# Kernel optimization log

Hardware: AMD Instinct MI355X
Metric: run time of the kernel (lower is better)

Reference implementation:

```python
import jax, jax.numpy as jnp
import numpy as np

NUM_MIXTURES = 10
DIM_INPUT = 512
DIM_FEATURES = 512
SEQ_LEN = 512
BATCH = 16
NUM_CHAR = 1024
DIM_CONTEXT = 256


def setup_inputs() -> dict:
    key = jax.random.key(0)
    ks = jax.random.split(key, 6)
    inputs = jax.random.normal(ks[0], (SEQ_LEN, BATCH, DIM_INPUT), dtype=jnp.float32)
    context_vectors = jax.random.normal(ks[1], (NUM_CHAR, BATCH, DIM_CONTEXT), dtype=jnp.float32)
    init_means = jnp.zeros((BATCH, NUM_MIXTURES), dtype=jnp.float32)
    # StackedLinearLayers params: 2 layers, leaky_relu between, out dim = 3*K
    s1 = 1.0 / np.sqrt(DIM_INPUT)
    s2 = 1.0 / np.sqrt(DIM_FEATURES)
    W1 = jax.random.uniform(ks[2], (DIM_INPUT, DIM_FEATURES), jnp.float32, -s1, s1)
    b1 = jax.random.uniform(ks[3], (DIM_FEATURES,), jnp.float32, -s1, s1)
    W2 = jax.random.uniform(ks[4], (DIM_FEATURES, 3 * NUM_MIXTURES), jnp.float32, -s2, s2)
    b2 = jax.random.uniform(ks[5], (3 * NUM_MIXTURES,), jnp.float32, -s2, s2)
    return dict(inputs=inputs, context_vectors=context_vectors, init_means=init_means,
                W1=W1, b1=b1, W2=W2, b2=b2, extra_chars=0)


def reference(inputs, context_vectors, init_means, W1, b1, W2, b2, extra_chars):
    K = NUM_MIXTURES
    seq_len, batch, _ = inputs.shape
    num_char = context_vectors.shape[0]
    total_char = num_char + extra_chars

    # StackedLinearLayers: leaky_relu MLP, last layer linear -> (S, B, 3K)
    h = jax.nn.leaky_relu(inputs @ W1 + b1, negative_slope=0.01)
    outs = h @ W2 + b2
    outs = jax.nn.softplus(outs)  # pos_fun = softplus

    delta_means, vars_, weights = jnp.split(outs, 3, axis=2)  # each (S, B, K)
    delta_means = delta_means / 25.0
    vars_ = jnp.clip(vars_, 0.01, 100.0)
    means = jnp.cumsum(delta_means, axis=0) + init_means[None, :, :]  # (S, B, K)

    cidxs = jnp.arange(total_char, dtype=jnp.float32)  # (T,)
    # dists: (S, B, K, T)
    dists = -((means[..., None] - cidxs) ** 2) * vars_[..., None]
    # attn_weights = exp(logsumexp over mixtures)
    attn_weights = jnp.exp(
        jax.scipy.special.logsumexp(jnp.log(weights)[..., None] + dists, axis=2)
    )  # (S, B, T)

    # attended contexts: (S, B, D)
    attn_contexts = jnp.einsum('sbc,cbd->sbd', attn_weights[:, :, :num_char], context_vectors)
    return attn_contexts, attn_weights, means, vars_, weights
```

## Files before the change

### kernel.cpp

```cpp
#include <hip/hip_runtime.h>
#include <math.h>

#define S_LEN 512
#define BATCH 16
#define DIN   512
#define DF    512
#define NMIX  10
#define NCHAR 1024
#define DCTX  256
#define M_ROWS (S_LEN*BATCH)

#define OFF_CTXOUT 0
#define OFF_ATTN   (S_LEN*BATCH*DCTX)
#define OFF_MEANS  (OFF_ATTN + S_LEN*BATCH*NCHAR)
#define OFF_VARS   (OFF_MEANS + S_LEN*BATCH*NMIX)
#define OFF_WTS    (OFF_VARS  + S_LEN*BATCH*NMIX)

#define WS_HH    0
#define WS_W2T   (8u<<20)
#define WS_DM    (9u<<20)

typedef float    f32x16 __attribute__((ext_vector_type(16)));
typedef float    f32x4v __attribute__((ext_vector_type(4)));
typedef _Float16 f16x8  __attribute__((ext_vector_type(8)));

__device__ __forceinline__ unsigned short f2h(float x) {
    union { _Float16 h; unsigned short u; } cv;
    cv.h = (_Float16)x;
    return cv.u;
}
__device__ __forceinline__ ushort4 cvt4(float4 v) {
    ushort4 o; o.x = f2h(v.x); o.y = f2h(v.y); o.z = f2h(v.z); o.w = f2h(v.w);
    return o;
}
__device__ __forceinline__ void nt_store4(float* p, float a, float b, float c, float d) {
    f32x4v v; v.x = a; v.y = b; v.z = c; v.w = d;
    __builtin_nontemporal_store(v, (f32x4v*)p);
}


__global__ __launch_bounds__(256) void gemm1_kernel(
    const float* __restrict__ X, const float* __restrict__ W1,
    const float* __restrict__ b1, unsigned short* __restrict__ Hh,
    const float* __restrict__ W2, float* __restrict__ W2T)
{
    const int tid = threadIdx.x;
    if (blockIdx.x >= 512) {
        const int base = (blockIdx.x - 512) * 4096 + tid;
        #pragma unroll
        for (int i = 0; i < 16; i++) {
            const int idx = base + i*256;
            const int j = idx >> 9, k = idx & 511;
            W2T[idx] = (j < 30) ? W2[k*30 + j] : 0.f;
        }
        return;
    }
    __shared__ __align__(16) unsigned short As[64*64];
    __shared__ __align__(16) unsigned short Bs[128*64];
    const int row0 = (blockIdx.x >> 2) * 64;
    const int n0   = (blockIdx.x & 3)  * 128;
    const int lane = tid & 63, w = tid >> 6;
    const int wr = (w >> 1) * 32, wc = (w & 1) * 64;
    const int m  = lane & 31,  g  = lane >> 5;
    const int sa = tid >> 2, ka = (tid & 3) * 16;
    const int kb = tid & 63, nq = (tid >> 6) * 32;

    f32x16 acc0 = {}, acc1 = {};
    const float* aptr = X + (size_t)(row0 + sa)*DIN + ka;
    const int sza = (sa & 7) << 3;
    const int szm = (m  & 7) << 3;

    for (int kt = 0; kt < DIN; kt += 64) {
        float4 a0 = *(const float4*)(aptr + kt + 0);
        float4 a1 = *(const float4*)(aptr + kt + 4);
        float4 a2 = *(const float4*)(aptr + kt + 8);
        float4 a3 = *(const float4*)(aptr + kt + 12);
        const float* bp = W1 + (size_t)(kt + kb)*DF + n0 + nq;
        float4 bv[8];
        #pragma unroll
        for (int u = 0; u < 8; u++) bv[u] = *(const float4*)(bp + u*4);
        __syncthreads();
        {
            union { ushort4 h[4]; uint4 q[2]; } ta;
            ta.h[0] = cvt4(a0); ta.h[1] = cvt4(a1);
            ta.h[2] = cvt4(a2); ta.h[3] = cvt4(a3);
            *(uint4*)(As + sa*64 + ( ka      ^ sza)) = ta.q[0];
            *(uint4*)(As + sa*64 + ((ka + 8) ^ sza)) = ta.q[1];
        }
        {
            const int cb = (kb & ~7), cs = (kb & 7);
            #pragma unroll
            for (int u = 0; u < 8; u++) {
                ushort4 h = cvt4(bv[u]);
                const int n = nq + u*4;
                Bs[(n+0)*64 + (cb ^ (((n+0)&7)<<3)) + cs] = h.x;
                Bs[(n+1)*64 + (cb ^ (((n+1)&7)<<3)) + cs] = h.y;
                Bs[(n+2)*64 + (cb ^ (((n+2)&7)<<3)) + cs] = h.z;
                Bs[(n+3)*64 + (cb ^ (((n+3)&7)<<3)) + cs] = h.w;
            }
        }
        __syncthreads();
        #pragma unroll
        for (int ks = 0; ks < 64; ks += 16) {
            const int ac = ks + g*8;
            f16x8 af  = *(const f16x8*)(As + (wr+m)*64      + (ac ^ szm));
            f16x8 bf0 = *(const f16x8*)(Bs + (wc+m)*64      + (ac ^ szm));
            f16x8 bf1 = *(const f16x8*)(Bs + (wc+32+m)*64   + (ac ^ szm));
            acc0 = __builtin_amdgcn_mfma_f32_32x32x16_f16(af, bf0, acc0, 0, 0, 0);
            acc1 = __builtin_amdgcn_mfma_f32_32x32x16_f16(af, bf1, acc1, 0, 0, 0);
        }
    }
    const int nc0 = n0 + wc + m;
    const float bb0 = b1[nc0], bb1 = b1[nc0 + 32];
    #pragma unroll
    for (int r = 0; r < 16; r++) {
        const int rowloc = (r & 3) + 8*(r >> 2) + 4*g;
        const int row = row0 + wr + rowloc;
        float v0 = acc0[r] + bb0;
        float v1 = acc1[r] + bb1;
        v0 = v0 > 0.f ? v0 : 0.01f * v0;
        v1 = v1 > 0.f ? v1 : 0.01f * v1;
        Hh[(size_t)row*DF + nc0]      = f2h(v0);
        Hh[(size_t)row*DF + nc0 + 32] = f2h(v1);
    }
}

__global__ __launch_bounds__(256) void gemm2_kernel(
    const unsigned short* __restrict__ Hh, const float* __restrict__ W2T,
    const float* __restrict__ b2,
    float* __restrict__ dm_ws, float* __restrict__ dvars, float* __restrict__ dwts)
{
    __shared__ __align__(16) unsigned short Hs[32*520];
    const int tid = threadIdx.x;
    const int r0  = blockIdx.x * 32;
    {
        const uint4* src = (const uint4*)(Hh + (size_t)r0*DF);
        #pragma unroll
        for (int i = 0; i < 8; i++) {
            int u   = tid + i*256;
            int row = u >> 6;
            int col = (u & 63) * 8;
            *(uint4*)(Hs + row*520 + col) = src[u];
        }
    }
    __syncthreads();

    const int r  = tid & 31;
    const int j0 = tid >> 5;
    const unsigned short* hrow = Hs + r*520;
    float acc[4] = {0.f, 0.f, 0.f, 0.f};

    for (int k0 = 0; k0 < DF; k0 += 8) {
        union { uint4 u; _Float16 h[8]; } hv;
        hv.u = *(const uint4*)(hrow + k0);
        float wv[4][8];
        #pragma unroll
        for (int q = 0; q < 4; q++) {
            *(float4*)(wv[q])     = *(const float4*)(W2T + (size_t)(j0 + q*8)*DF + k0);
            *(float4*)(wv[q] + 4) = *(const float4*)(W2T + (size_t)(j0 + q*8)*DF + k0 + 4);
        }
        #pragma unroll
        for (int i = 0; i < 8; i++) {
            float hf = (float)hv.h[i];
            acc[0] = fmaf(hf, wv[0][i], acc[0]);
            acc[1] = fmaf(hf, wv[1][i], acc[1]);
            acc[2] = fmaf(hf, wv[2][i], acc[2]);
            acc[3] = fmaf(hf, wv[3][i], acc[3]);
        }
    }
    const int row = r0 + r;
    #pragma unroll
    for (int q = 0; q < 4; q++) {
        const int j = j0 + q*8;
        if (j >= 30) continue;
        float dot = acc[q] + b2[j];
        float sp  = fmaxf(dot, 0.f) + log1pf(__expf(-fabsf(dot)));
        if (j < 10) {
            const int bb = row & (BATCH-1), s = row >> 4;
            dm_ws[((size_t)bb*NMIX + j)*S_LEN + s] = sp * (1.f/25.f);
        }
        else if (j < 20)  dvars[row*NMIX + (j-10)] = fminf(fmaxf(sp, 0.01f), 100.f);
        else              dwts [row*NMIX + (j-20)] = sp;
    }
}

__global__ __launch_bounds__(512) void fused_kernel(
    const float* __restrict__ dm_ws, const float* __restrict__ init_means,
    const float* __restrict__ vars_g, const float* __restrict__ wts_g,
    const float* __restrict__ ctx,
    float* __restrict__ means_out, float* __restrict__ attn_out,
    float* __restrict__ ctxout)
{
    __shared__ float mlds[320];
    __shared__ float vlds[320];
    __shared__ float wlds[320];
    __shared__ float redbuf[8];
    __shared__ __align__(16) unsigned short As[32*64];
    __shared__ __align__(16) unsigned short Bs[256*64];

    const int bid = blockIdx.x;
    const int b   = bid >> 4;
    const int s0  = (bid & 15) * 32;
    const int tid = threadIdx.x;
    const int lane = tid & 63, w = tid >> 6;
    const int m = lane & 31, g = lane >> 5;

    const int send = s0 + 32;
    for (int k = w; k < NMIX; k += 8) {
        float carry = init_means[b*NMIX + k];
        const float* chain = dm_ws + ((size_t)b*NMIX + k)*S_LEN;
        for (int sseg = 0; sseg < send; sseg += 64) {
            const int s = sseg + lane;
            float v = (s < send) ? chain[s] : 0.f;
            #pragma unroll
            for (int d = 1; d < 64; d <<= 1) {
                float t = __shfl_up(v, d, 64);
                if (lane >= d) v += t;
            }
            const float x = v + carry;
            carry = __shfl(x, 63, 64);
            if (s >= s0 && s < send) mlds[(s - s0)*NMIX + k] = x;
        }
    }
    if (tid < 320) {
        const int s = tid / NMIX, k = tid - s*NMIX;
        const int row = (s0 + s)*BATCH + b;
        vlds[tid] = vars_g[row*NMIX + k];
        wlds[tid] = wts_g [row*NMIX + k];
    }
    __syncthreads();

    float reach = 0.f;
    if (tid < 320) {
        const int s = tid / NMIX, k = tid - s*NMIX;
        means_out[((s0 + s)*BATCH + b)*NMIX + k] = mlds[tid];
        reach = mlds[tid] + 4.8f * rsqrtf(vlds[tid]);
    }
    #pragma unroll
    for (int d = 32; d >= 1; d >>= 1) reach = fmaxf(reach, __shfl_xor(reach, d, 64));
    if (lane == 0) redbuf[w] = reach;
    __syncthreads();
    float rmax = redbuf[0];
    #pragma unroll
    for (int i = 1; i < 8; i++) rmax = fmaxf(rmax, redbuf[i]);
    const int kmax = min(NCHAR, (((int)rmax) + 64) & ~63);

    const int r  = tid >> 4;
    const int ti = tid & 15;
    float mr[NMIX], vr[NMIX], wr_[NMIX];
    #pragma unroll
    for (int k = 0; k < NMIX; k++) {
        mr[k] = mlds[r*NMIX + k];
        vr[k] = vlds[r*NMIX + k];
        wr_[k] = wlds[r*NMIX + k];
    }
    const size_t arow = (size_t)((s0 + r)*BATCH + b) * NCHAR;

    const int tb = tid & 63, dq = tid >> 6;
    const float* cbase = ctx + (size_t)b*DCTX + dq*32;
    const int szm = (m & 7) << 3;

    f32x16 acc = {};
    for (int kt = 0; kt < kmax; kt += 64) {
        float o[4];
        #pragma unroll
        for (int i = 0; i < 4; i++) {
            const float t = (float)(kt + ti*4 + i);
            float sum = 0.f;
            #pragma unroll
            for (int k = 0; k < NMIX; k++) {
                float d = t - mr[k];
                sum += wr_[k] * __expf(-d*d*vr[k]);
            }
            o[i] = sum;
        }
        float4 cf[8];
        #pragma unroll
        for (int u = 0; u < 8; u++)
            cf[u] = *(const float4*)(cbase + (size_t)(kt + tb)*(BATCH*DCTX) + u*4);
        __syncthreads();
        nt_store4(attn_out + arow + kt + ti*4, o[0], o[1], o[2], o[3]);
        {
            ushort4 h; h.x = f2h(o[0]); h.y = f2h(o[1]); h.z = f2h(o[2]); h.w = f2h(o[3]);
            const int c = ti*4;
            *(ushort4*)(As + r*64 + ((c & ~7) ^ ((r&7)<<3)) + (c & 7)) = h;
        }
        {
            const int cb = (tb & ~7), cs = (tb & 7);
            #pragma unroll
            for (int u = 0; u < 8; u++) {
                ushort4 h = cvt4(cf[u]);
                const int n = dq*32 + u*4;
                Bs[(n+0)*64 + (cb ^ (((n+0)&7)<<3)) + cs] = h.x;
                Bs[(n+1)*64 + (cb ^ (((n+1)&7)<<3)) + cs] = h.y;
                Bs[(n+2)*64 + (cb ^ (((n+2)&7)<<3)) + cs] = h.z;
                Bs[(n+3)*64 + (cb ^ (((n+3)&7)<<3)) + cs] = h.w;
            }
        }
        __syncthreads();
        #pragma unroll
        for (int ks = 0; ks < 64; ks += 16) {
            const int ac = ks + g*8;
            f16x8 af = *(const f16x8*)(As + m*64 + (ac ^ szm));
            const int brow = w*32 + m;
            f16x8 bf = *(const f16x8*)(Bs + brow*64 + (ac ^ ((brow&7)<<3)));
            acc = __builtin_amdgcn_mfma_f32_32x32x16_f16(af, bf, acc, 0, 0, 0);
        }
    }
    for (int t = kmax + ti*4; t < NCHAR; t += 64)
        nt_store4(attn_out + arow + t, 0.f, 0.f, 0.f, 0.f);

    #pragma unroll
    for (int rr = 0; rr < 16; rr++) {
        const int rowloc = (rr & 3) + 8*(rr >> 2) + 4*g;
        const int s = s0 + rowloc;
        __builtin_nontemporal_store(acc[rr],
            ctxout + ((size_t)s*BATCH + b)*DCTX + w*32 + m);
    }
}

extern "C" void kernel_launch(void* const* d_in, const int* in_sizes, int n_in,
                              void* d_out, int out_size, void* d_ws, size_t ws_size,
                              hipStream_t stream)
{
    const float* X     = (const float*)d_in[0];
    const float* ctx   = (const float*)d_in[1];
    const float* initm = (const float*)d_in[2];
    const float* W1    = (const float*)d_in[3];
    const float* b1    = (const float*)d_in[4];
    const float* W2    = (const float*)d_in[5];
    const float* b2    = (const float*)d_in[6];

    float* out      = (float*)d_out;
    float* out_ctx  = out + OFF_CTXOUT;
    float* out_attn = out + OFF_ATTN;
    float* out_mean = out + OFF_MEANS;
    float* out_var  = out + OFF_VARS;
    float* out_wts  = out + OFF_WTS;

    char* ws = (char*)d_ws;
    unsigned short* Hh   = (unsigned short*)(ws + WS_HH);
    float*          W2T  = (float*)         (ws + WS_W2T);
    float*          dmws = (float*)         (ws + WS_DM);

    gemm1_kernel<<<512 + 4, 256, 0, stream>>>(X, W1, b1, Hh, W2, W2T);
    gemm2_kernel<<<M_ROWS/32, 256, 0, stream>>>(Hh, W2T, b2, dmws, out_var, out_wts);
    fused_kernel<<<BATCH*16, 512, 0, stream>>>(dmws, initm, out_var, out_wts, ctx,
                                               out_mean, out_attn, out_ctx);
}
```

Baseline: 149.7 us.

## Fuse MLP GEMMs into one kernel with pre-transposed fp16 W1

Adds a small pre-pass that converts W1 to fp16 and transposes it, along with W2. The two MLP layers are merged into a single kernel: each block computes a full 32x512 hidden tile in LDS and immediately applies the second layer, so the fp16 hidden matrix never goes to global memory. The cumsum in the fused kernel is also rewritten as a block-prefix reduction plus a 32-wide scan instead of a serial segmented scan. In exchange, each block now reloads the whole W1T slice (512x64 per k-step), which raises L2 traffic, and larger LDS use may lower occupancy.

```diff
diff --git a/kernel.cpp b/kernel.cpp
--- a/kernel.cpp
+++ b/kernel.cpp
@@ -16,9 +16,9 @@
 #define OFF_VARS   (OFF_MEANS + S_LEN*BATCH*NMIX)
 #define OFF_WTS    (OFF_VARS  + S_LEN*BATCH*NMIX)
 
-#define WS_HH    0
-#define WS_W2T   (8u<<20)
-#define WS_DM    (9u<<20)
+#define WS_W1T   0
+#define WS_W2T   (1u<<20)
+#define WS_DM    (2u<<20)
 
 typedef float    f32x16 __attribute__((ext_vector_type(16)));
 typedef float    f32x4v __attribute__((ext_vector_type(4)));
@@ -38,142 +38,130 @@
     __builtin_nontemporal_store(v, (f32x4v*)p);
 }
 
-
-__global__ __launch_bounds__(256) void gemm1_kernel(
-    const float* __restrict__ X, const float* __restrict__ W1,
-    const float* __restrict__ b1, unsigned short* __restrict__ Hh,
-    const float* __restrict__ W2, float* __restrict__ W2T)
+__global__ __launch_bounds__(256) void convert_kernel(
+    const float* __restrict__ W1, const float* __restrict__ W2,
+    unsigned short* __restrict__ W1T, float* __restrict__ W2T)
 {
+    const int bid = blockIdx.x;
     const int tid = threadIdx.x;
-    if (blockIdx.x >= 512) {
-        const int base = (blockIdx.x - 512) * 4096 + tid;
-        #pragma unroll
-        for (int i = 0; i < 16; i++) {
-            const int idx = base + i*256;
-            const int j = idx >> 9, k = idx & 511;
-            W2T[idx] = (j < 30) ? W2[k*30 + j] : 0.f;
-        }
-        return;
-    }
-    __shared__ __align__(16) unsigned short As[64*64];
-    __shared__ __align__(16) unsigned short Bs[128*64];
-    const int row0 = (blockIdx.x >> 2) * 64;
-    const int n0   = (blockIdx.x & 3)  * 128;
+    if (bid < 64) {
+        __shared__ unsigned short tile[64*68];
+        const int k0 = (bid >> 3) * 64, n0 = (bid & 7) * 64;
+        #pragma unroll
+        for (int q = 0; q < 4; q++) {
+            const int r = q*16 + (tid >> 4);
+            const int c = (tid & 15) * 4;
+            float4 v = *(const float4*)(W1 + (size_t)(k0+r)*DF + n0 + c);
+            *(ushort4*)(tile + r*68 + c) = cvt4(v);
+        }
+        __syncthreads();
+        #pragma unroll
+        for (int q = 0; q < 4; q++) {
+            const int n  = q*16 + (tid >> 4);
+            const int kq = (tid & 15) * 4;
+            ushort4 o;
+            o.x = tile[(kq+0)*68 + n];
+            o.y = tile[(kq+1)*68 + n];
+            o.z = tile[(kq+2)*68 + n];
+            o.w = tile[(kq+3)*68 + n];
+            *(ushort4*)(W1T + (size_t)(n0+n)*DIN + k0 + kq) = o;
+        }
+    } else {
+        const int idx = (bid - 64)*256 + tid;
+        const int j = idx >> 9, k = idx & 511;
+        W2T[idx] = (j < 30) ? W2[k*30 + j] : 0.f;
+    }
+}
+
+__global__ __launch_bounds__(512) void gemm12_kernel(
+    const float* __restrict__ X, const unsigned short* __restrict__ W1T,
+    const float* __restrict__ b1,
+    const float* __restrict__ W2T, const float* __restrict__ b2,
+    float* __restrict__ dm_ws, float* __restrict__ dvars, float* __restrict__ dwts)
+{
+    __shared__ __align__(16) unsigned short As[32*64];
+    __shared__ __align__(16) unsigned short Bs[512*64];
+    const int tid  = threadIdx.x;
+    const int r0   = blockIdx.x * 32;
     const int lane = tid & 63, w = tid >> 6;
-    const int wr = (w >> 1) * 32, wc = (w & 1) * 64;
-    const int m  = lane & 31,  g  = lane >> 5;
-    const int sa = tid >> 2, ka = (tid & 3) * 16;
-    const int kb = tid & 63, nq = (tid >> 6) * 32;
+    const int m = lane & 31, g = lane >> 5;
+    const int ra = tid >> 4, c4 = (tid & 15) * 4;
+    const int sza = (ra & 7) << 3;
+    const int nb0 = tid >> 3, cb = (tid & 7) * 8;
+    const int szm = (m & 7) << 3;
 
     f32x16 acc0 = {}, acc1 = {};
-    const float* aptr = X + (size_t)(row0 + sa)*DIN + ka;
-    const int sza = (sa & 7) << 3;
-    const int szm = (m  & 7) << 3;
+    const float* aptr = X + (size_t)(r0 + ra)*DIN + c4;
 
     for (int kt = 0; kt < DIN; kt += 64) {
-        float4 a0 = *(const float4*)(aptr + kt + 0);
-        float4 a1 = *(const float4*)(aptr + kt + 4);
-        float4 a2 = *(const float4*)(aptr + kt + 8);
-        float4 a3 = *(const float4*)(aptr + kt + 12);
-        const float* bp = W1 + (size_t)(kt + kb)*DF + n0 + nq;
-        float4 bv[8];
-        #pragma unroll
-        for (int u = 0; u < 8; u++) bv[u] = *(const float4*)(bp + u*4);
+        float4 av = *(const float4*)(aptr + kt);
+        uint4 bv[8];
+        #pragma unroll
+        for (int u = 0; u < 8; u++)
+            bv[u] = *(const uint4*)(W1T + (size_t)(nb0 + u*64)*DIN + kt + cb);
         __syncthreads();
         {
-            union { ushort4 h[4]; uint4 q[2]; } ta;
-            ta.h[0] = cvt4(a0); ta.h[1] = cvt4(a1);
-            ta.h[2] = cvt4(a2); ta.h[3] = cvt4(a3);
-            *(uint4*)(As + sa*64 + ( ka      ^ sza)) = ta.q[0];
-            *(uint4*)(As + sa*64 + ((ka + 8) ^ sza)) = ta.q[1];
-        }
-        {
-            const int cb = (kb & ~7), cs = (kb & 7);
-            #pragma unroll
-            for (int u = 0; u < 8; u++) {
-                ushort4 h = cvt4(bv[u]);
-                const int n = nq + u*4;
-                Bs[(n+0)*64 + (cb ^ (((n+0)&7)<<3)) + cs] = h.x;
-                Bs[(n+1)*64 + (cb ^ (((n+1)&7)<<3)) + cs] = h.y;
-                Bs[(n+2)*64 + (cb ^ (((n+2)&7)<<3)) + cs] = h.z;
-                Bs[(n+3)*64 + (cb ^ (((n+3)&7)<<3)) + cs] = h.w;
-            }
+            ushort4 h = cvt4(av);
+            *(ushort4*)(As + ra*64 + (((c4 & ~7) ^ sza)) + (c4 & 7)) = h;
+        }
+        #pragma unroll
+        for (int u = 0; u < 8; u++) {
+            const int n = nb0 + u*64;
+            *(uint4*)(Bs + n*64 + (cb ^ ((n & 7) << 3))) = bv[u];
         }
         __syncthreads();
         #pragma unroll
         for (int ks = 0; ks < 64; ks += 16) {
             const int ac = ks + g*8;
-            f16x8 af  = *(const f16x8*)(As + (wr+m)*64      + (ac ^ szm));
-            f16x8 bf0 = *(const f16x8*)(Bs + (wc+m)*64      + (ac ^ szm));
-            f16x8 bf1 = *(const f16x8*)(Bs + (wc+32+m)*64   + (ac ^ szm));
+            f16x8 af  = *(const f16x8*)(As + m*64 + (ac ^ szm));
+            f16x8 bf0 = *(const f16x8*)(Bs + (w*64 + m)*64      + (ac ^ szm));
+            f16x8 bf1 = *(const f16x8*)(Bs + (w*64 + 32 + m)*64 + (ac ^ szm));
             acc0 = __builtin_amdgcn_mfma_f32_32x32x16_f16(af, bf0, acc0, 0, 0, 0);
             acc1 = __builtin_amdgcn_mfma_f32_32x32x16_f16(af, bf1, acc1, 0, 0, 0);
         }
     }
-    const int nc0 = n0 + wc + m;
-    const float bb0 = b1[nc0], bb1 = b1[nc0 + 32];
-    #pragma unroll
-    for (int r = 0; r < 16; r++) {
-        const int rowloc = (r & 3) + 8*(r >> 2) + 4*g;
-        const int row = row0 + wr + rowloc;
-        float v0 = acc0[r] + bb0;
-        float v1 = acc1[r] + bb1;
-        v0 = v0 > 0.f ? v0 : 0.01f * v0;
-        v1 = v1 > 0.f ? v1 : 0.01f * v1;
-        Hh[(size_t)row*DF + nc0]      = f2h(v0);
-        Hh[(size_t)row*DF + nc0 + 32] = f2h(v1);
-    }
-}
-
-__global__ __launch_bounds__(256) void gemm2_kernel(
-    const unsigned short* __restrict__ Hh, const float* __restrict__ W2T,
-    const float* __restrict__ b2,
-    float* __restrict__ dm_ws, float* __restrict__ dvars, float* __restrict__ dwts)
-{
-    __shared__ __align__(16) unsigned short Hs[32*520];
-    const int tid = threadIdx.x;
-    const int r0  = blockIdx.x * 32;
+    __syncthreads();
+    unsigned short* Hs = Bs;
     {
-        const uint4* src = (const uint4*)(Hh + (size_t)r0*DF);
-        #pragma unroll
-        for (int i = 0; i < 8; i++) {
-            int u   = tid + i*256;
-            int row = u >> 6;
-            int col = (u & 63) * 8;
-            *(uint4*)(Hs + row*520 + col) = src[u];
+        const int nc0 = w*64 + m;
+        const float bb0 = b1[nc0], bb1 = b1[nc0 + 32];
+        #pragma unroll
+        for (int r = 0; r < 16; r++) {
+            const int rowloc = (r & 3) + 8*(r >> 2) + 4*g;
+            float v0 = acc0[r] + bb0;
+            float v1 = acc1[r] + bb1;
+            v0 = v0 > 0.f ? v0 : 0.01f*v0;
+            v1 = v1 > 0.f ? v1 : 0.01f*v1;
+            Hs[rowloc*520 + nc0]      = f2h(v0);
+            Hs[rowloc*520 + nc0 + 32] = f2h(v1);
         }
     }
     __syncthreads();
-
-    const int r  = tid & 31;
-    const int j0 = tid >> 5;
+    const int r = tid & 31, j0 = tid >> 5;
     const unsigned short* hrow = Hs + r*520;
-    float acc[4] = {0.f, 0.f, 0.f, 0.f};
-
+    float a2[2] = {0.f, 0.f};
     for (int k0 = 0; k0 < DF; k0 += 8) {
         union { uint4 u; _Float16 h[8]; } hv;
         hv.u = *(const uint4*)(hrow + k0);
-        float wv[4][8];
-        #pragma unroll
-        for (int q = 0; q < 4; q++) {
-            *(float4*)(wv[q])     = *(const float4*)(W2T + (size_t)(j0 + q*8)*DF + k0);
-            *(float4*)(wv[q] + 4) = *(const float4*)(W2T + (size_t)(j0 + q*8)*DF + k0 + 4);
+        float wv[2][8];
+        #pragma unroll
+        for (int q = 0; q < 2; q++) {
+            *(float4*)(wv[q])     = *(const float4*)(W2T + (size_t)(j0 + q*16)*DF + k0);
+            *(float4*)(wv[q] + 4) = *(const float4*)(W2T + (size_t)(j0 + q*16)*DF + k0 + 4);
         }
         #pragma unroll
         for (int i = 0; i < 8; i++) {
             float hf = (float)hv.h[i];
-            acc[0] = fmaf(hf, wv[0][i], acc[0]);
-            acc[1] = fmaf(hf, wv[1][i], acc[1]);
-            acc[2] = fmaf(hf, wv[2][i], acc[2]);
-            acc[3] = fmaf(hf, wv[3][i], acc[3]);
+            a2[0] = fmaf(hf, wv[0][i], a2[0]);
+            a2[1] = fmaf(hf, wv[1][i], a2[1]);
         }
     }
     const int row = r0 + r;
     #pragma unroll
-    for (int q = 0; q < 4; q++) {
-        const int j = j0 + q*8;
+    for (int q = 0; q < 2; q++) {
+        const int j = j0 + q*16;
         if (j >= 30) continue;
-        float dot = acc[q] + b2[j];
+        float dot = a2[q] + b2[j];
         float sp  = fmaxf(dot, 0.f) + log1pf(__expf(-fabsf(dot)));
         if (j < 10) {
             const int bb = row & (BATCH-1), s = row >> 4;
@@ -205,22 +193,20 @@
     const int lane = tid & 63, w = tid >> 6;
     const int m = lane & 31, g = lane >> 5;
 
-    const int send = s0 + 32;
     for (int k = w; k < NMIX; k += 8) {
-        float carry = init_means[b*NMIX + k];
         const float* chain = dm_ws + ((size_t)b*NMIX + k)*S_LEN;
-        for (int sseg = 0; sseg < send; sseg += 64) {
-            const int s = sseg + lane;
-            float v = (s < send) ? chain[s] : 0.f;
-            #pragma unroll
-            for (int d = 1; d < 64; d <<= 1) {
-                float t = __shfl_up(v, d, 64);
-                if (lane >= d) v += t;
-            }
-            const float x = v + carry;
-            carry = __shfl(x, 63, 64);
-            if (s >= s0 && s < send) mlds[(s - s0)*NMIX + k] = x;
-        }
+        float part = 0.f;
+        for (int s = lane; s < s0; s += 64) part += chain[s];
+        #pragma unroll
+        for (int d = 32; d >= 1; d >>= 1) part += __shfl_xor(part, d, 64);
+        const float carry = init_means[b*NMIX + k] + part;
+        float v = (lane < 32) ? chain[s0 + lane] : 0.f;
+        #pragma unroll
+        for (int d = 1; d < 32; d <<= 1) {
+            float t = __shfl_up(v, d, 64);
+            if (lane >= d) v += t;
+        }
+        if (lane < 32) mlds[lane*NMIX + k] = carry + v;
     }
     if (tid < 320) {
         const int s = tid / NMIX, k = tid - s*NMIX;
@@ -339,12 +325,13 @@
     float* out_wts  = out + OFF_WTS;
 
     char* ws = (char*)d_ws;
-    unsigned short* Hh   = (unsigned short*)(ws + WS_HH);
+    unsigned short* W1T  = (unsigned short*)(ws + WS_W1T);
     float*          W2T  = (float*)         (ws + WS_W2T);
     float*          dmws = (float*)         (ws + WS_DM);
 
-    gemm1_kernel<<<512 + 4, 256, 0, stream>>>(X, W1, b1, Hh, W2, W2T);
-    gemm2_kernel<<<M_ROWS/32, 256, 0, stream>>>(Hh, W2T, b2, dmws, out_var, out_wts);
+    convert_kernel<<<128, 256, 0, stream>>>(W1, W2, W1T, W2T);
+    gemm12_kernel<<<M_ROWS/32, 512, 0, stream>>>(X, W1T, b1, W2T, b2,
+                                                 dmws, out_var, out_wts);
     fused_kernel<<<BATCH*16, 512, 0, stream>>>(dmws, initm, out_var, out_wts, ctx,
                                                out_mean, out_attn, out_ctx);
 }
```

Result: slower. 175.2 us (+17.0%).
